# Performance work log

Measured on AMD Instinct MI355X. Metric: run time of the kernel, lower is better.

Reference implementation:

```python
import jax, jax.numpy as jnp
import numpy as np

N_NODES = 200000
N_EDGES = 400000
N_FEAT = 78
DIM = 128
N_LAYERS = 5
N_GRAPHS = 8192
BN_EPS = 1e-5


def setup_inputs() -> dict:
    key = jax.random.key(0)
    ks = jax.random.split(key, 20)
    s = 0.05
    inp = {
        "x": jax.random.normal(ks[0], (N_NODES, N_FEAT), dtype=jnp.float32),
        "edge_index": jax.random.randint(ks[1], (2, N_EDGES), 0, N_NODES, dtype=jnp.int64),
        "batch": jnp.sort(jax.random.randint(ks[2], (N_NODES,), 0, N_GRAPHS, dtype=jnp.int64)),
        "percent": 0,
        # ini_embed: Linear(F,D), ReLU, Linear(D,D)
        "ini_w1": jax.random.normal(ks[3], (N_FEAT, DIM), dtype=jnp.float32) * s,
        "ini_b1": jnp.zeros((DIM,), dtype=jnp.float32),
        "ini_w2": jax.random.normal(ks[4], (DIM, DIM), dtype=jnp.float32) * s,
        "ini_b2": jnp.zeros((DIM,), dtype=jnp.float32),
        # per-layer GIN MLPs (stacked over layers)
        "gin_w1": jax.random.normal(ks[5], (N_LAYERS, DIM, DIM), dtype=jnp.float32) * s,
        "gin_b1": jnp.zeros((N_LAYERS, DIM), dtype=jnp.float32),
        "gin_w2": jax.random.normal(ks[6], (N_LAYERS, DIM, DIM), dtype=jnp.float32) * s,
        "gin_b2": jnp.zeros((N_LAYERS, DIM), dtype=jnp.float32),
        # BatchNorm1d params per layer
        "bn_gamma": jnp.ones((N_LAYERS, DIM), dtype=jnp.float32),
        "bn_beta": jnp.zeros((N_LAYERS, DIM), dtype=jnp.float32),
        # layer_conv: Conv2d(L, 1, (1,1)) == weighted sum over layer axis + scalar bias
        "lc_w": jax.random.normal(ks[7], (N_LAYERS,), dtype=jnp.float32) * s,
        "lc_b": jnp.zeros((), dtype=jnp.float32),
    }
    return inp


def reference(x, edge_index, batch, percent, ini_w1, ini_b1, ini_w2, ini_b2,
              gin_w1, gin_b1, gin_w2, gin_b2, bn_gamma, bn_beta, lc_w, lc_b):
    # ini_embed
    h = jax.nn.relu(x @ ini_w1 + ini_b1) @ ini_w2 + ini_b2  # [N, D]
    src, dst = edge_index[0], edge_index[1]

    layer_outs = []
    for i in range(N_LAYERS):
        # GINConv (eps=0): mlp(x_i + sum_{j->i} x_j)
        agg = jax.ops.segment_sum(h[src], dst, num_segments=N_NODES)  # scatter-add
        z = agg + h
        z = jax.nn.relu(z @ gin_w1[i] + gin_b1[i]) @ gin_w2[i] + gin_b2[i]
        z = jax.nn.relu(z)
        # BatchNorm1d (training-mode batch stats over nodes)
        mean = jnp.mean(z, axis=0)
        var = jnp.var(z, axis=0)
        z = (z - mean) * jax.lax.rsqrt(var + BN_EPS) * bn_gamma[i] + bn_beta[i]
        layer_outs.append(z)
        h = z

    stacked = jnp.stack(layer_outs, axis=1)  # [N, L, D]
    # layer_conv: 1x1 Conv2d over the layer channel axis
    pos_global_node = jnp.einsum('nld,l->nd', stacked, lc_w) + lc_b  # [N, D]
    # global_add_pool
    pos_global_graph = jax.ops.segment_sum(pos_global_node, batch, num_segments=N_GRAPHS)
    return pos_global_graph
```

## Files before the change

### kernel.cpp

```cpp
#include <hip/hip_runtime.h>

#define NN 200000
#define NE 400000
#define NFEAT 78
#define DIM 128
#define NLAYERS 5
#define NGRAPHS 8192
#define BN_EPS_C 1e-5f
#define NSLOT 32

typedef __attribute__((ext_vector_type(8))) short short8;
typedef __attribute__((ext_vector_type(8))) unsigned short ushort8;
typedef __attribute__((ext_vector_type(4))) float f32x4;

__device__ inline float bf2f(unsigned short u) {
    union { unsigned int i; float f; } c; c.i = ((unsigned int)u) << 16; return c.f;
}
__device__ inline unsigned short f2bf(float f) {
    union { float f; unsigned int i; } c; c.f = f;
    unsigned int x = c.i;
    x += 0x7FFFu + ((x >> 16) & 1u);
    return (unsigned short)(x >> 16);
}

template<int RELU2, int STATS>
__global__ __launch_bounds__(256, 4) void gin_mlp_kernel(
    const unsigned short* __restrict__ A,
    const unsigned short* __restrict__ W1d, const unsigned short* __restrict__ W2d,
    const float* __restrict__ b1, const float* __restrict__ b2,
    unsigned short* __restrict__ Z, float* __restrict__ stats_base)
{
    __shared__ unsigned short C1[128 * 128];

    int t = threadIdx.x;
    int r0 = blockIdx.x * 128;
    int lane = t & 63;
    int wv = t >> 6;
    int l15 = lane & 15;
    int lg = lane >> 4;

    float b1v[8], b2v[8];
#pragma unroll
    for (int nt = 0; nt < 8; ++nt) { b1v[nt] = b1[nt * 16 + l15]; b2v[nt] = b2[nt * 16 + l15]; }

    int ra0 = r0 + wv * 32 + l15;       if (ra0 > NN - 1) ra0 = NN - 1;
    int ra1 = r0 + wv * 32 + 16 + l15;  if (ra1 > NN - 1) ra1 = NN - 1;
    const unsigned short* __restrict__ Arow0 = A + (size_t)ra0 * DIM;
    const unsigned short* __restrict__ Arow1 = A + (size_t)ra1 * DIM;

    f32x4 zero4 = {0.f, 0.f, 0.f, 0.f};
    f32x4 acc[2][8];
#pragma unroll
    for (int mt = 0; mt < 2; ++mt)
#pragma unroll
        for (int nt = 0; nt < 8; ++nt) acc[mt][nt] = zero4;

#pragma unroll
    for (int ks = 0; ks < 4; ++ks) {
        int kgp = ks * 4 + lg;
        short8 a0 = *(const short8*)(Arow0 + kgp * 8);
        short8 a1 = *(const short8*)(Arow1 + kgp * 8);
#pragma unroll
        for (int nt = 0; nt < 8; ++nt) {
            short8 b = *(const short8*)(W1d + (size_t)(kgp * 128 + nt * 16 + l15) * 8);
            acc[0][nt] = __builtin_amdgcn_mfma_f32_16x16x32_bf16(a0, b, acc[0][nt], 0, 0, 0);
            acc[1][nt] = __builtin_amdgcn_mfma_f32_16x16x32_bf16(a1, b, acc[1][nt], 0, 0, 0);
        }
    }

#pragma unroll
    for (int mt = 0; mt < 2; ++mt)
#pragma unroll
        for (int nt = 0; nt < 8; ++nt)
#pragma unroll
            for (int rg = 0; rg < 4; ++rg) {
                int rr = wv * 32 + mt * 16 + lg * 4 + rg;
                int c = nt * 16 + l15;
                float v = fmaxf(acc[mt][nt][rg] + b1v[nt], 0.f);
                unsigned byte = (unsigned)((rr * 128 + c) * 2) ^ (unsigned)((rr & 7) << 4);
                *(unsigned short*)((char*)C1 + byte) = f2bf(v);
            }

    f32x4 acc2[2][8];
#pragma unroll
    for (int mt = 0; mt < 2; ++mt)
#pragma unroll
        for (int nt = 0; nt < 8; ++nt) acc2[mt][nt] = zero4;

#pragma unroll
    for (int ks = 0; ks < 4; ++ks) {
        int kgp = ks * 4 + lg;
        int m0 = wv * 32 + l15, m1 = m0 + 16;
        unsigned ba0 = (unsigned)(m0 * 256 + kgp * 16) ^ (unsigned)((m0 & 7) << 4);
        unsigned ba1 = (unsigned)(m1 * 256 + kgp * 16) ^ (unsigned)((m1 & 7) << 4);
        short8 a0 = *(const short8*)((char*)C1 + ba0);
        short8 a1 = *(const short8*)((char*)C1 + ba1);
#pragma unroll
        for (int nt = 0; nt < 8; ++nt) {
            short8 b = *(const short8*)(W2d + (size_t)(kgp * 128 + nt * 16 + l15) * 8);
            acc2[0][nt] = __builtin_amdgcn_mfma_f32_16x16x32_bf16(a0, b, acc2[0][nt], 0, 0, 0);
            acc2[1][nt] = __builtin_amdgcn_mfma_f32_16x16x32_bf16(a1, b, acc2[1][nt], 0, 0, 0);
        }
    }

#pragma unroll
    for (int nt = 0; nt < 8; ++nt) {
        float sum8 = 0.f, sq8 = 0.f;
        int c = nt * 16 + l15;
#pragma unroll
        for (int mt = 0; mt < 2; ++mt)
#pragma unroll
            for (int rg = 0; rg < 4; ++rg) {
                int rr = wv * 32 + mt * 16 + lg * 4 + rg;
                int r = r0 + rr;
                if (r < NN) {
                    float v = acc2[mt][nt][rg] + b2v[nt];
                    if (RELU2) v = fmaxf(v, 0.f);
                    Z[(size_t)r * DIM + c] = f2bf(v);
                    if (STATS) { sum8 += v; sq8 += v * v; }
                }
            }
        if (STATS) {
            sum8 += __shfl_xor(sum8, 16); sum8 += __shfl_xor(sum8, 32);
            sq8  += __shfl_xor(sq8, 16);  sq8  += __shfl_xor(sq8, 32);
            if (lg == 0) {
                float* sb = stats_base + (size_t)(blockIdx.x & (NSLOT - 1)) * 256;
                atomicAdd(&sb[c], sum8);
                atomicAdd(&sb[128 + c], sq8);
            }
        }
    }
}

__global__ __launch_bounds__(256) void wconv_kernel(
    const float* __restrict__ ini_w1, const float* __restrict__ ini_w2,
    const float* __restrict__ gw1, const float* __restrict__ gw2,
    unsigned short* __restrict__ Wd)
{
    int id = blockIdx.x * 256 + threadIdx.x;
    int k = id >> 7, n = id & 127;
    int y = blockIdx.y;
    float v;
    if (y == 0)      v = (k < NFEAT) ? ini_w1[k * DIM + n] : 0.f;
    else if (y == 1) v = ini_w2[k * DIM + n];
    else if (y < 7)  v = gw1[(size_t)(y - 2) * DIM * DIM + k * DIM + n];
    else             v = gw2[(size_t)(y - 7) * DIM * DIM + k * DIM + n];
    int kg = k >> 3;
    Wd[(size_t)y * 16384 + (size_t)(kg * 128 + n) * 8 + (k & 7)] = f2bf(v);
}

__global__ __launch_bounds__(256) void xpad_kernel(
    const float* __restrict__ x, unsigned short* __restrict__ xp)
{
    int t = blockIdx.x * 256 + threadIdx.x;
    int n = t >> 4, j = t & 15;
    ushort8 o;
#pragma unroll
    for (int i = 0; i < 8; ++i) {
        int c = j * 8 + i;
        o[i] = (c < NFEAT) ? f2bf(x[(size_t)n * NFEAT + c]) : (unsigned short)0;
    }
    *(ushort8*)(xp + (size_t)n * DIM + j * 8) = o;
}

__global__ __launch_bounds__(256) void deg_kernel(const int* __restrict__ ei, int* __restrict__ deg)
{
    int e = blockIdx.x * 256 + threadIdx.x;
    if (e >= NE) return;
    atomicAdd(&deg[ei[NE + e]], 1);
}

__global__ __launch_bounds__(256) void scanA_kernel(
    const int* __restrict__ deg, int* __restrict__ cursor, int* __restrict__ partials)
{
    __shared__ int sh[256];
    int i = blockIdx.x * 256 + threadIdx.x;
    int v = (i < NN) ? deg[i] : 0;
    sh[threadIdx.x] = v;
    __syncthreads();
    for (int off = 1; off < 256; off <<= 1) {
        int t2 = (threadIdx.x >= off) ? sh[threadIdx.x - off] : 0;
        __syncthreads();
        sh[threadIdx.x] += t2;
        __syncthreads();
    }
    int incl = sh[threadIdx.x];
    if (i < NN) cursor[i] = incl - v;
    if (threadIdx.x == 255) partials[blockIdx.x] = incl;
}

__global__ __launch_bounds__(1024) void scanB_kernel(int* __restrict__ partials, int nb)
{
    __shared__ int sh[1024];
    int i = threadIdx.x;
    int v = (i < nb) ? partials[i] : 0;
    sh[i] = v;
    __syncthreads();
    for (int off = 1; off < 1024; off <<= 1) {
        int t2 = (i >= off) ? sh[i - off] : 0;
        __syncthreads();
        sh[i] += t2;
        __syncthreads();
    }
    if (i < nb) partials[i] = sh[i] - v;
}

__global__ __launch_bounds__(256) void scanC_kernel(
    int* __restrict__ cursor, const int* __restrict__ partials)
{
    int i = blockIdx.x * 256 + threadIdx.x;
    if (i < NN) cursor[i] += partials[blockIdx.x];
}

__global__ __launch_bounds__(256) void fill_kernel(
    const int* __restrict__ ei, int* __restrict__ cursor, int* __restrict__ csr_src)
{
    int e = blockIdx.x * 256 + threadIdx.x;
    if (e >= NE) return;
    int slot = atomicAdd(&cursor[ei[NE + e]], 1);
    csr_src[slot] = ei[e];
}

__global__ __launch_bounds__(256) void gptr_kernel(
    const int* __restrict__ batch, int* __restrict__ gptr)
{
    int n = blockIdx.x * 256 + threadIdx.x;
    if (n > NN) return;
    int b1 = (n < NN) ? batch[n] : NGRAPHS;
    int b0 = (n == 0) ? -1 : batch[n - 1];
    for (int g = b0 + 1; g <= b1; ++g) gptr[g] = n;
}

__global__ void ident_kernel(float* __restrict__ aff)
{
    int d = threadIdx.x;
    aff[d] = 1.f;
    aff[DIM + d] = 0.f;
}

__global__ __launch_bounds__(256) void gather_kernel(
    const unsigned short* __restrict__ z, const int* __restrict__ cursor,
    const int* __restrict__ csr_src, const float* __restrict__ aff,
    unsigned short* __restrict__ agg)
{
    int t = blockIdx.x * 256 + threadIdx.x;
    int n = t >> 4, j = t & 15;
    int end = cursor[n];
    int beg = (n == 0) ? 0 : cursor[n - 1];
    ushort8 sv = *(const ushort8*)(z + (size_t)n * DIM + j * 8);
    float a[8];
#pragma unroll
    for (int i = 0; i < 8; ++i) a[i] = bf2f(sv[i]);
    for (int e = beg; e < end; ++e) {
        int s = csr_src[e];
        ushort8 v = *(const ushort8*)(z + (size_t)s * DIM + j * 8);
#pragma unroll
        for (int i = 0; i < 8; ++i) a[i] += bf2f(v[i]);
    }
    float cnt = (float)(end - beg + 1);
    ushort8 o;
#pragma unroll
    for (int i = 0; i < 8; ++i) {
        float av = aff[j * 8 + i];
        float cv = aff[DIM + j * 8 + i];
        o[i] = f2bf(fmaf(av, a[i], cnt * cv));
    }
    *(ushort8*)(agg + (size_t)n * DIM + j * 8) = o;
}

__global__ __launch_bounds__(128) void pool_kernel(
    const unsigned short* __restrict__ z, const int* __restrict__ gptr,
    const float* __restrict__ aff, const float* __restrict__ lcw, int l,
    const float* __restrict__ lcb_p, int add_lcb, float* __restrict__ out)
{
    int g = blockIdx.x;
    int d = threadIdx.x;
    int p0 = gptr[g], p1 = gptr[g + 1];
    float S = 0.f;
    for (int n = p0; n < p1; ++n) S += bf2f(z[(size_t)n * DIM + d]);
    float w = lcw[l];
    float cnt = (float)(p1 - p0);
    float v = w * fmaf(aff[d], S, cnt * aff[DIM + d]);
    if (add_lcb) v = fmaf(cnt, *lcb_p, v);
    out[(size_t)g * DIM + d] += v;
}

__global__ void finalize_kernel(
    const float* __restrict__ slots, const float* __restrict__ gamma,
    const float* __restrict__ beta, float* __restrict__ aff)
{
    int d = threadIdx.x;
    float s = 0.f, sq = 0.f;
    for (int i = 0; i < NSLOT; ++i) {
        s  += slots[i * 256 + d];
        sq += slots[i * 256 + 128 + d];
    }
    float mean = s * (1.0f / NN);
    float var = sq * (1.0f / NN) - mean * mean;
    float a = gamma[d] * rsqrtf(var + BN_EPS_C);
    aff[d] = a;
    aff[DIM + d] = beta[d] - mean * a;
}

extern "C" void kernel_launch(void* const* d_in, const int* in_sizes, int n_in,
                              void* d_out, int out_size, void* d_ws, size_t ws_size,
                              hipStream_t stream)
{
    const float* x      = (const float*)d_in[0];
    const int*   ei     = (const int*)d_in[1];
    const int*   batch  = (const int*)d_in[2];
    const float* ini_w1 = (const float*)d_in[4];
    const float* ini_b1 = (const float*)d_in[5];
    const float* ini_w2 = (const float*)d_in[6];
    const float* ini_b2 = (const float*)d_in[7];
    const float* gw1    = (const float*)d_in[8];
    const float* gb1    = (const float*)d_in[9];
    const float* gw2    = (const float*)d_in[10];
    const float* gb2    = (const float*)d_in[11];
    const float* gamma  = (const float*)d_in[12];
    const float* beta   = (const float*)d_in[13];
    const float* lcw    = (const float*)d_in[14];
    const float* lcb    = (const float*)d_in[15];
    float* out = (float*)d_out;

    size_t NHs = (size_t)NN * DIM;
    unsigned short* bufA = (unsigned short*)d_ws;
    unsigned short* bufB = bufA + NHs;
    unsigned short* Wd   = bufB + NHs;
    float* stats  = (float*)(Wd + 12 * 16384);
    float* affine = stats + (size_t)NLAYERS * NSLOT * 256;
    int* deg      = (int*)(affine + (NLAYERS + 1) * 256);
    int* cursor   = deg + NN;
    int* csr_src  = cursor + NN;
    int* partials = csr_src + NE;
    int* gptr     = partials + 1024;
    size_t need = (size_t)((char*)(gptr + NGRAPHS + 1) - (char*)d_ws);

    hipMemsetAsync(out, 0, (size_t)NGRAPHS * DIM * sizeof(float), stream);
    if (ws_size < need) return;

    hipMemsetAsync(stats, 0, (size_t)NLAYERS * NSLOT * 256 * sizeof(float), stream);
    hipMemsetAsync(deg, 0, NN * sizeof(int), stream);

    int nb = (NN + 255) / 256;
    int eb = (NE + 255) / 256;

    deg_kernel<<<eb, 256, 0, stream>>>(ei, deg);
    scanA_kernel<<<nb, 256, 0, stream>>>(deg, cursor, partials);
    scanB_kernel<<<1, 1024, 0, stream>>>(partials, nb);
    scanC_kernel<<<nb, 256, 0, stream>>>(cursor, partials);
    fill_kernel<<<eb, 256, 0, stream>>>(ei, cursor, csr_src);
    gptr_kernel<<<(NN + 256) / 256 + 1, 256, 0, stream>>>(batch, gptr);
    ident_kernel<<<1, 128, 0, stream>>>(affine);

    xpad_kernel<<<NN * 16 / 256, 256, 0, stream>>>(x, bufB);
    wconv_kernel<<<dim3(64, 12), 256, 0, stream>>>(ini_w1, ini_w2, gw1, gw2, Wd);

    int gin_blocks = (NN + 127) / 128;

    gin_mlp_kernel<0, 0><<<gin_blocks, 256, 0, stream>>>(
        bufB, Wd, Wd + 16384, ini_b1, ini_b2, bufA, nullptr);

    unsigned short* prev = bufA;
    for (int l = 0; l < NLAYERS; ++l) {
        unsigned short* nxt = (prev == bufA) ? bufB : bufA;
        gather_kernel<<<NN * 16 / 256, 256, 0, stream>>>(
            prev, cursor, csr_src, affine + (size_t)l * 256, nxt);
        gin_mlp_kernel<1, 1><<<gin_blocks, 256, 0, stream>>>(
            nxt, Wd + (size_t)(2 + l) * 16384, Wd + (size_t)(7 + l) * 16384,
            gb1 + l * DIM, gb2 + l * DIM, nxt, stats + (size_t)l * NSLOT * 256);
        finalize_kernel<<<1, 128, 0, stream>>>(
            stats + (size_t)l * NSLOT * 256, gamma + l * DIM, beta + l * DIM,
            affine + (size_t)(l + 1) * 256);
        pool_kernel<<<NGRAPHS, 128, 0, stream>>>(
            nxt, gptr, affine + (size_t)(l + 1) * 256, lcw, l, lcb,
            (l == 0) ? 1 : 0, out);
        prev = nxt;
    }
}
```

Baseline: 754.5 us.

## Fuse neighbor gather into GIN MLP kernel with LDS-staged coalesced stores

The separate gather kernel is removed. Each MLP block now computes the neighbor aggregation and BN affine for its 128-row tile directly into shared memory and feeds it to the first MFMA GEMM. This avoids writing and re-reading the aggregated bf16 activations in global memory every layer. The output tile is also staged through the swizzled LDS buffer so the final stores are 16-byte coalesced. Each block processes two tiles, so fewer blocks run and the irregular gather latency is no longer overlapped by a separate, highly parallel kernel.

```diff
diff --git a/kernel.cpp b/kernel.cpp
--- a/kernel.cpp
+++ b/kernel.cpp
@@ -8,6 +8,7 @@
 #define NGRAPHS 8192
 #define BN_EPS_C 1e-5f
 #define NSLOT 32
+#define NTILES 1563
 
 typedef __attribute__((ext_vector_type(8))) short short8;
 typedef __attribute__((ext_vector_type(8))) unsigned short ushort8;
@@ -23,17 +24,18 @@
     return (unsigned short)(x >> 16);
 }
 
-template<int RELU2, int STATS>
-__global__ __launch_bounds__(256, 4) void gin_mlp_kernel(
+template<int GATHERM, int RELU2, int STATS>
+__global__ __launch_bounds__(256, 4) void gin_fused_kernel(
     const unsigned short* __restrict__ A,
+    const int* __restrict__ cursor, const int* __restrict__ csr_src,
+    const float* __restrict__ aff,
     const unsigned short* __restrict__ W1d, const unsigned short* __restrict__ W2d,
     const float* __restrict__ b1, const float* __restrict__ b2,
     unsigned short* __restrict__ Z, float* __restrict__ stats_base)
 {
-    __shared__ unsigned short C1[128 * 128];
+    __shared__ unsigned short S[128 * 128];
 
     int t = threadIdx.x;
-    int r0 = blockIdx.x * 128;
     int lane = t & 63;
     int wv = t >> 6;
     int l15 = lane & 15;
@@ -43,90 +45,156 @@
 #pragma unroll
     for (int nt = 0; nt < 8; ++nt) { b1v[nt] = b1[nt * 16 + l15]; b2v[nt] = b2[nt * 16 + l15]; }
 
-    int ra0 = r0 + wv * 32 + l15;       if (ra0 > NN - 1) ra0 = NN - 1;
-    int ra1 = r0 + wv * 32 + 16 + l15;  if (ra1 > NN - 1) ra1 = NN - 1;
-    const unsigned short* __restrict__ Arow0 = A + (size_t)ra0 * DIM;
-    const unsigned short* __restrict__ Arow1 = A + (size_t)ra1 * DIM;
-
-    f32x4 zero4 = {0.f, 0.f, 0.f, 0.f};
-    f32x4 acc[2][8];
-#pragma unroll
-    for (int mt = 0; mt < 2; ++mt)
-#pragma unroll
-        for (int nt = 0; nt < 8; ++nt) acc[mt][nt] = zero4;
-
-#pragma unroll
-    for (int ks = 0; ks < 4; ++ks) {
-        int kgp = ks * 4 + lg;
-        short8 a0 = *(const short8*)(Arow0 + kgp * 8);
-        short8 a1 = *(const short8*)(Arow1 + kgp * 8);
+    float av[8], cv[8];
+    if (GATHERM) {
+        int j = t & 15;
+#pragma unroll
+        for (int i = 0; i < 8; ++i) { av[i] = aff[j * 8 + i]; cv[i] = aff[DIM + j * 8 + i]; }
+    }
+
+    for (int tile = blockIdx.x * 2; tile < blockIdx.x * 2 + 2; ++tile) {
+        if (tile >= NTILES) break;
+        int r0 = tile * 128;
+
+        if (GATHERM) {
+            if (tile != blockIdx.x * 2) __syncthreads();
+            int j = t & 15;
+#pragma unroll
+            for (int it = 0; it < 8; ++it) {
+                int lr = it * 16 + (t >> 4);
+                int n = r0 + lr;
+                ushort8 o;
+                if (n < NN) {
+                    int end = cursor[n];
+                    int beg = (n == 0) ? 0 : cursor[n - 1];
+                    ushort8 sv = *(const ushort8*)(A + (size_t)n * DIM + j * 8);
+                    float acc[8];
+#pragma unroll
+                    for (int i = 0; i < 8; ++i) acc[i] = bf2f(sv[i]);
+                    for (int e = beg; e < end; ++e) {
+                        int s = csr_src[e];
+                        ushort8 v = *(const ushort8*)(A + (size_t)s * DIM + j * 8);
+#pragma unroll
+                        for (int i = 0; i < 8; ++i) acc[i] += bf2f(v[i]);
+                    }
+                    float cnt = (float)(end - beg + 1);
+#pragma unroll
+                    for (int i = 0; i < 8; ++i) o[i] = f2bf(fmaf(av[i], acc[i], cnt * cv[i]));
+                } else {
+#pragma unroll
+                    for (int i = 0; i < 8; ++i) o[i] = 0;
+                }
+                unsigned byte = (unsigned)(lr * 256 + j * 16) ^ (unsigned)((lr & 7) << 4);
+                *(ushort8*)((char*)S + byte) = o;
+            }
+            __syncthreads();
+        }
+
+        int ra0 = r0 + wv * 32 + l15;       if (ra0 > NN - 1) ra0 = NN - 1;
+        int ra1 = r0 + wv * 32 + 16 + l15;  if (ra1 > NN - 1) ra1 = NN - 1;
+        const unsigned short* Arow0 = A + (size_t)ra0 * DIM;
+        const unsigned short* Arow1 = A + (size_t)ra1 * DIM;
+
+        f32x4 zero4 = {0.f, 0.f, 0.f, 0.f};
+        f32x4 acc[2][8];
+#pragma unroll
+        for (int mt = 0; mt < 2; ++mt)
+#pragma unroll
+            for (int nt = 0; nt < 8; ++nt) acc[mt][nt] = zero4;
+
+#pragma unroll
+        for (int ks = 0; ks < 4; ++ks) {
+            int kgp = ks * 4 + lg;
+            short8 a0, a1;
+            if (GATHERM) {
+                int m0 = wv * 32 + l15, m1 = m0 + 16;
+                unsigned ba0 = (unsigned)(m0 * 256 + kgp * 16) ^ (unsigned)((m0 & 7) << 4);
+                unsigned ba1 = (unsigned)(m1 * 256 + kgp * 16) ^ (unsigned)((m1 & 7) << 4);
+                a0 = *(const short8*)((char*)S + ba0);
+                a1 = *(const short8*)((char*)S + ba1);
+            } else {
+                a0 = *(const short8*)(Arow0 + kgp * 8);
+                a1 = *(const short8*)(Arow1 + kgp * 8);
+            }
+#pragma unroll
+            for (int nt = 0; nt < 8; ++nt) {
+                short8 b = *(const short8*)(W1d + (size_t)(kgp * 128 + nt * 16 + l15) * 8);
+                acc[0][nt] = __builtin_amdgcn_mfma_f32_16x16x32_bf16(a0, b, acc[0][nt], 0, 0, 0);
+                acc[1][nt] = __builtin_amdgcn_mfma_f32_16x16x32_bf16(a1, b, acc[1][nt], 0, 0, 0);
+            }
+        }
+
+#pragma unroll
+        for (int mt = 0; mt < 2; ++mt)
+#pragma unroll
+            for (int nt = 0; nt < 8; ++nt)
+#pragma unroll
+                for (int rg = 0; rg < 4; ++rg) {
+                    int rr = wv * 32 + mt * 16 + lg * 4 + rg;
+                    int c = nt * 16 + l15;
+                    float v = fmaxf(acc[mt][nt][rg] + b1v[nt], 0.f);
+                    unsigned byte = (unsigned)(rr * 256 + c * 2) ^ (unsigned)((rr & 7) << 4);
+                    *(unsigned short*)((char*)S + byte) = f2bf(v);
+                }
+
+        f32x4 acc2[2][8];
+#pragma unroll
+        for (int mt = 0; mt < 2; ++mt)
+#pragma unroll
+            for (int nt = 0; nt < 8; ++nt) acc2[mt][nt] = zero4;
+
+#pragma unroll
+        for (int ks = 0; ks < 4; ++ks) {
+            int kgp = ks * 4 + lg;
+            int m0 = wv * 32 + l15, m1 = m0 + 16;
+            unsigned ba0 = (unsigned)(m0 * 256 + kgp * 16) ^ (unsigned)((m0 & 7) << 4);
+            unsigned ba1 = (unsigned)(m1 * 256 + kgp * 16) ^ (unsigned)((m1 & 7) << 4);
+            short8 a0 = *(const short8*)((char*)S + ba0);
+            short8 a1 = *(const short8*)((char*)S + ba1);
+#pragma unroll
+            for (int nt = 0; nt < 8; ++nt) {
+                short8 b = *(const short8*)(W2d + (size_t)(kgp * 128 + nt * 16 + l15) * 8);
+                acc2[0][nt] = __builtin_amdgcn_mfma_f32_16x16x32_bf16(a0, b, acc2[0][nt], 0, 0, 0);
+                acc2[1][nt] = __builtin_amdgcn_mfma_f32_16x16x32_bf16(a1, b, acc2[1][nt], 0, 0, 0);
+            }
+        }
+
 #pragma unroll
         for (int nt = 0; nt < 8; ++nt) {
-            short8 b = *(const short8*)(W1d + (size_t)(kgp * 128 + nt * 16 + l15) * 8);
-            acc[0][nt] = __builtin_amdgcn_mfma_f32_16x16x32_bf16(a0, b, acc[0][nt], 0, 0, 0);
-            acc[1][nt] = __builtin_amdgcn_mfma_f32_16x16x32_bf16(a1, b, acc[1][nt], 0, 0, 0);
-        }
-    }
-
-#pragma unroll
-    for (int mt = 0; mt < 2; ++mt)
-#pragma unroll
-        for (int nt = 0; nt < 8; ++nt)
-#pragma unroll
-            for (int rg = 0; rg < 4; ++rg) {
-                int rr = wv * 32 + mt * 16 + lg * 4 + rg;
-                int c = nt * 16 + l15;
-                float v = fmaxf(acc[mt][nt][rg] + b1v[nt], 0.f);
-                unsigned byte = (unsigned)((rr * 128 + c) * 2) ^ (unsigned)((rr & 7) << 4);
-                *(unsigned short*)((char*)C1 + byte) = f2bf(v);
-            }
-
-    f32x4 acc2[2][8];
-#pragma unroll
-    for (int mt = 0; mt < 2; ++mt)
-#pragma unroll
-        for (int nt = 0; nt < 8; ++nt) acc2[mt][nt] = zero4;
-
-#pragma unroll
-    for (int ks = 0; ks < 4; ++ks) {
-        int kgp = ks * 4 + lg;
-        int m0 = wv * 32 + l15, m1 = m0 + 16;
-        unsigned ba0 = (unsigned)(m0 * 256 + kgp * 16) ^ (unsigned)((m0 & 7) << 4);
-        unsigned ba1 = (unsigned)(m1 * 256 + kgp * 16) ^ (unsigned)((m1 & 7) << 4);
-        short8 a0 = *(const short8*)((char*)C1 + ba0);
-        short8 a1 = *(const short8*)((char*)C1 + ba1);
-#pragma unroll
-        for (int nt = 0; nt < 8; ++nt) {
-            short8 b = *(const short8*)(W2d + (size_t)(kgp * 128 + nt * 16 + l15) * 8);
-            acc2[0][nt] = __builtin_amdgcn_mfma_f32_16x16x32_bf16(a0, b, acc2[0][nt], 0, 0, 0);
-            acc2[1][nt] = __builtin_amdgcn_mfma_f32_16x16x32_bf16(a1, b, acc2[1][nt], 0, 0, 0);
-        }
-    }
-
-#pragma unroll
-    for (int nt = 0; nt < 8; ++nt) {
-        float sum8 = 0.f, sq8 = 0.f;
-        int c = nt * 16 + l15;
-#pragma unroll
-        for (int mt = 0; mt < 2; ++mt)
-#pragma unroll
-            for (int rg = 0; rg < 4; ++rg) {
-                int rr = wv * 32 + mt * 16 + lg * 4 + rg;
-                int r = r0 + rr;
-                if (r < NN) {
+            float sum8 = 0.f, sq8 = 0.f;
+            int c = nt * 16 + l15;
+#pragma unroll
+            for (int mt = 0; mt < 2; ++mt)
+#pragma unroll
+                for (int rg = 0; rg < 4; ++rg) {
+                    int rr = wv * 32 + mt * 16 + lg * 4 + rg;
                     float v = acc2[mt][nt][rg] + b2v[nt];
                     if (RELU2) v = fmaxf(v, 0.f);
-                    Z[(size_t)r * DIM + c] = f2bf(v);
-                    if (STATS) { sum8 += v; sq8 += v * v; }
+                    unsigned byte = (unsigned)(rr * 256 + c * 2) ^ (unsigned)((rr & 7) << 4);
+                    *(unsigned short*)((char*)S + byte) = f2bf(v);
+                    if (STATS && (r0 + rr < NN)) { sum8 += v; sq8 += v * v; }
                 }
-            }
-        if (STATS) {
-            sum8 += __shfl_xor(sum8, 16); sum8 += __shfl_xor(sum8, 32);
-            sq8  += __shfl_xor(sq8, 16);  sq8  += __shfl_xor(sq8, 32);
-            if (lg == 0) {
-                float* sb = stats_base + (size_t)(blockIdx.x & (NSLOT - 1)) * 256;
-                atomicAdd(&sb[c], sum8);
-                atomicAdd(&sb[128 + c], sq8);
+            if (STATS) {
+                sum8 += __shfl_xor(sum8, 16); sum8 += __shfl_xor(sum8, 32);
+                sq8  += __shfl_xor(sq8, 16);  sq8  += __shfl_xor(sq8, 32);
+                if (lg == 0) {
+                    float* sb = stats_base + (size_t)(tile & (NSLOT - 1)) * 256;
+                    atomicAdd(&sb[c], sum8);
+                    atomicAdd(&sb[128 + c], sq8);
+                }
+            }
+        }
+
+#pragma unroll
+        for (int st = 0; st < 8; ++st) {
+            int idx = st * 64 + lane;
+            int lr2 = wv * 32 + (idx >> 4);
+            int j2 = idx & 15;
+            int r = r0 + lr2;
+            if (r < NN) {
+                unsigned byte = (unsigned)(lr2 * 256 + j2 * 16) ^ (unsigned)((lr2 & 7) << 4);
+                ushort8 v = *(const ushort8*)((char*)S + byte);
+                *(ushort8*)(Z + (size_t)r * DIM + j2 * 8) = v;
             }
         }
     }
@@ -236,36 +304,6 @@
     int d = threadIdx.x;
     aff[d] = 1.f;
     aff[DIM + d] = 0.f;
-}
-
-__global__ __launch_bounds__(256) void gather_kernel(
-    const unsigned short* __restrict__ z, const int* __restrict__ cursor,
-    const int* __restrict__ csr_src, const float* __restrict__ aff,
-    unsigned short* __restrict__ agg)
-{
-    int t = blockIdx.x * 256 + threadIdx.x;
-    int n = t >> 4, j = t & 15;
-    int end = cursor[n];
-    int beg = (n == 0) ? 0 : cursor[n - 1];
-    ushort8 sv = *(const ushort8*)(z + (size_t)n * DIM + j * 8);
-    float a[8];
-#pragma unroll
-    for (int i = 0; i < 8; ++i) a[i] = bf2f(sv[i]);
-    for (int e = beg; e < end; ++e) {
-        int s = csr_src[e];
-        ushort8 v = *(const ushort8*)(z + (size_t)s * DIM + j * 8);
-#pragma unroll
-        for (int i = 0; i < 8; ++i) a[i] += bf2f(v[i]);
-    }
-    float cnt = (float)(end - beg + 1);
-    ushort8 o;
-#pragma unroll
-    for (int i = 0; i < 8; ++i) {
-        float av = aff[j * 8 + i];
-        float cv = aff[DIM + j * 8 + i];
-        o[i] = f2bf(fmaf(av, a[i], cnt * cv));
-    }
-    *(ushort8*)(agg + (size_t)n * DIM + j * 8) = o;
 }
 
 __global__ __launch_bounds__(128) void pool_kernel(
@@ -356,18 +394,17 @@
     xpad_kernel<<<NN * 16 / 256, 256, 0, stream>>>(x, bufB);
     wconv_kernel<<<dim3(64, 12), 256, 0, stream>>>(ini_w1, ini_w2, gw1, gw2, Wd);
 
-    int gin_blocks = (NN + 127) / 128;
-
-    gin_mlp_kernel<0, 0><<<gin_blocks, 256, 0, stream>>>(
-        bufB, Wd, Wd + 16384, ini_b1, ini_b2, bufA, nullptr);
+    int fused_blocks = (NTILES + 1) / 2;
+
+    gin_fused_kernel<0, 0, 0><<<fused_blocks, 256, 0, stream>>>(
+        bufB, nullptr, nullptr, nullptr, Wd, Wd + 16384, ini_b1, ini_b2, bufA, nullptr);
 
     unsigned short* prev = bufA;
     for (int l = 0; l < NLAYERS; ++l) {
         unsigned short* nxt = (prev == bufA) ? bufB : bufA;
-        gather_kernel<<<NN * 16 / 256, 256, 0, stream>>>(
-            prev, cursor, csr_src, affine + (size_t)l * 256, nxt);
-        gin_mlp_kernel<1, 1><<<gin_blocks, 256, 0, stream>>>(
-            nxt, Wd + (size_t)(2 + l) * 16384, Wd + (size_t)(7 + l) * 16384,
+        gin_fused_kernel<1, 1, 1><<<fused_blocks, 256, 0, stream>>>(
+            prev, cursor, csr_src, affine + (size_t)l * 256,
+            Wd + (size_t)(2 + l) * 16384, Wd + (size_t)(7 + l) * 16384,
             gb1 + l * DIM, gb2 + l * DIM, nxt, stats + (size_t)l * NSLOT * 256);
         finalize_kernel<<<1, 128, 0, stream>>>(
             stats + (size_t)l * NSLOT * 256, gamma + l * DIM, beta + l * DIM,
```

After: 2.555 ms. 3.39x slower.

## Restructure GIN MLP kernel to single-wave blocks with LDS-staged vector stores

Applied to the files above, without the earlier changes.

Each fused two-layer MLP block now holds one 64-thread wave that handles 32 rows as two sequential 16-row tiles, instead of four waves over 128 rows. The shared intermediate buffer shrinks from 32KB to 4KB, and accumulator register pressure is halved, which should allow more resident blocks per CU. Output is staged through swizzled LDS and written with 16-byte vector stores rather than scattered 2-byte stores. The trade-offs are more blocks to schedule, more atomics for BN statistics, and no bounds guard on rows, which relies on NN being a multiple of 32.

```diff
diff --git a/kernel.cpp b/kernel.cpp
--- a/kernel.cpp
+++ b/kernel.cpp
@@ -24,110 +24,103 @@
 }
 
 template<int RELU2, int STATS>
-__global__ __launch_bounds__(256, 4) void gin_mlp_kernel(
+__global__ __launch_bounds__(64, 6) void gin_mlp_kernel(
     const unsigned short* __restrict__ A,
     const unsigned short* __restrict__ W1d, const unsigned short* __restrict__ W2d,
     const float* __restrict__ b1, const float* __restrict__ b2,
     unsigned short* __restrict__ Z, float* __restrict__ stats_base)
 {
-    __shared__ unsigned short C1[128 * 128];
-
-    int t = threadIdx.x;
-    int r0 = blockIdx.x * 128;
-    int lane = t & 63;
-    int wv = t >> 6;
+    __shared__ unsigned short S[16 * 128];
+
+    int lane = threadIdx.x;
     int l15 = lane & 15;
     int lg = lane >> 4;
+    int r0 = blockIdx.x * 32;
 
     float b1v[8], b2v[8];
 #pragma unroll
     for (int nt = 0; nt < 8; ++nt) { b1v[nt] = b1[nt * 16 + l15]; b2v[nt] = b2[nt * 16 + l15]; }
 
-    int ra0 = r0 + wv * 32 + l15;       if (ra0 > NN - 1) ra0 = NN - 1;
-    int ra1 = r0 + wv * 32 + 16 + l15;  if (ra1 > NN - 1) ra1 = NN - 1;
-    const unsigned short* __restrict__ Arow0 = A + (size_t)ra0 * DIM;
-    const unsigned short* __restrict__ Arow1 = A + (size_t)ra1 * DIM;
-
     f32x4 zero4 = {0.f, 0.f, 0.f, 0.f};
-    f32x4 acc[2][8];
-#pragma unroll
-    for (int mt = 0; mt < 2; ++mt)
-#pragma unroll
-        for (int nt = 0; nt < 8; ++nt) acc[mt][nt] = zero4;
-
-#pragma unroll
-    for (int ks = 0; ks < 4; ++ks) {
-        int kgp = ks * 4 + lg;
-        short8 a0 = *(const short8*)(Arow0 + kgp * 8);
-        short8 a1 = *(const short8*)(Arow1 + kgp * 8);
+
+#pragma unroll
+    for (int mt = 0; mt < 2; ++mt) {
+        const unsigned short* __restrict__ Arow = A + (size_t)(r0 + mt * 16 + l15) * DIM;
+
+        f32x4 acc[8];
+#pragma unroll
+        for (int nt = 0; nt < 8; ++nt) acc[nt] = zero4;
+
+#pragma unroll
+        for (int ks = 0; ks < 4; ++ks) {
+            int kgp = ks * 4 + lg;
+            short8 a = *(const short8*)(Arow + kgp * 8);
+#pragma unroll
+            for (int nt = 0; nt < 8; ++nt) {
+                short8 b = *(const short8*)(W1d + (size_t)(kgp * 128 + nt * 16 + l15) * 8);
+                acc[nt] = __builtin_amdgcn_mfma_f32_16x16x32_bf16(a, b, acc[nt], 0, 0, 0);
+            }
+        }
+
+#pragma unroll
+        for (int nt = 0; nt < 8; ++nt)
+#pragma unroll
+            for (int rg = 0; rg < 4; ++rg) {
+                int lr = lg * 4 + rg;
+                int c = nt * 16 + l15;
+                float v = fmaxf(acc[nt][rg] + b1v[nt], 0.f);
+                unsigned byte = (unsigned)(lr * 256 + c * 2) ^ (unsigned)((lr & 7) << 4);
+                *(unsigned short*)((char*)S + byte) = f2bf(v);
+            }
+
+        f32x4 acc2[8];
+#pragma unroll
+        for (int nt = 0; nt < 8; ++nt) acc2[nt] = zero4;
+
+#pragma unroll
+        for (int ks = 0; ks < 4; ++ks) {
+            int kgp = ks * 4 + lg;
+            unsigned ba = (unsigned)(l15 * 256 + kgp * 16) ^ (unsigned)((l15 & 7) << 4);
+            short8 a = *(const short8*)((char*)S + ba);
+#pragma unroll
+            for (int nt = 0; nt < 8; ++nt) {
+                short8 b = *(const short8*)(W2d + (size_t)(kgp * 128 + nt * 16 + l15) * 8);
+                acc2[nt] = __builtin_amdgcn_mfma_f32_16x16x32_bf16(a, b, acc2[nt], 0, 0, 0);
+            }
+        }
+
 #pragma unroll
         for (int nt = 0; nt < 8; ++nt) {
-            short8 b = *(const short8*)(W1d + (size_t)(kgp * 128 + nt * 16 + l15) * 8);
-            acc[0][nt] = __builtin_amdgcn_mfma_f32_16x16x32_bf16(a0, b, acc[0][nt], 0, 0, 0);
-            acc[1][nt] = __builtin_amdgcn_mfma_f32_16x16x32_bf16(a1, b, acc[1][nt], 0, 0, 0);
+            float sum8 = 0.f, sq8 = 0.f;
+            int c = nt * 16 + l15;
+#pragma unroll
+            for (int rg = 0; rg < 4; ++rg) {
+                int lr = lg * 4 + rg;
+                float v = acc2[nt][rg] + b2v[nt];
+                if (RELU2) v = fmaxf(v, 0.f);
+                unsigned byte = (unsigned)(lr * 256 + c * 2) ^ (unsigned)((lr & 7) << 4);
+                *(unsigned short*)((char*)S + byte) = f2bf(v);
+                if (STATS) { sum8 += v; sq8 += v * v; }
+            }
+            if (STATS) {
+                sum8 += __shfl_xor(sum8, 16); sum8 += __shfl_xor(sum8, 32);
+                sq8  += __shfl_xor(sq8, 16);  sq8  += __shfl_xor(sq8, 32);
+                if (lg == 0) {
+                    float* sb = stats_base + (size_t)(blockIdx.x & (NSLOT - 1)) * 256;
+                    atomicAdd(&sb[c], sum8);
+                    atomicAdd(&sb[128 + c], sq8);
+                }
+            }
         }
-    }
-
-#pragma unroll
-    for (int mt = 0; mt < 2; ++mt)
-#pragma unroll
-        for (int nt = 0; nt < 8; ++nt)
-#pragma unroll
-            for (int rg = 0; rg < 4; ++rg) {
-                int rr = wv * 32 + mt * 16 + lg * 4 + rg;
-                int c = nt * 16 + l15;
-                float v = fmaxf(acc[mt][nt][rg] + b1v[nt], 0.f);
-                unsigned byte = (unsigned)((rr * 128 + c) * 2) ^ (unsigned)((rr & 7) << 4);
-                *(unsigned short*)((char*)C1 + byte) = f2bf(v);
-            }
-
-    f32x4 acc2[2][8];
-#pragma unroll
-    for (int mt = 0; mt < 2; ++mt)
-#pragma unroll
-        for (int nt = 0; nt < 8; ++nt) acc2[mt][nt] = zero4;
-
-#pragma unroll
-    for (int ks = 0; ks < 4; ++ks) {
-        int kgp = ks * 4 + lg;
-        int m0 = wv * 32 + l15, m1 = m0 + 16;
-        unsigned ba0 = (unsigned)(m0 * 256 + kgp * 16) ^ (unsigned)((m0 & 7) << 4);
-        unsigned ba1 = (unsigned)(m1 * 256 + kgp * 16) ^ (unsigned)((m1 & 7) << 4);
-        short8 a0 = *(const short8*)((char*)C1 + ba0);
-        short8 a1 = *(const short8*)((char*)C1 + ba1);
-#pragma unroll
-        for (int nt = 0; nt < 8; ++nt) {
-            short8 b = *(const short8*)(W2d + (size_t)(kgp * 128 + nt * 16 + l15) * 8);
-            acc2[0][nt] = __builtin_amdgcn_mfma_f32_16x16x32_bf16(a0, b, acc2[0][nt], 0, 0, 0);
-            acc2[1][nt] = __builtin_amdgcn_mfma_f32_16x16x32_bf16(a1, b, acc2[1][nt], 0, 0, 0);
-        }
-    }
-
-#pragma unroll
-    for (int nt = 0; nt < 8; ++nt) {
-        float sum8 = 0.f, sq8 = 0.f;
-        int c = nt * 16 + l15;
-#pragma unroll
-        for (int mt = 0; mt < 2; ++mt)
-#pragma unroll
-            for (int rg = 0; rg < 4; ++rg) {
-                int rr = wv * 32 + mt * 16 + lg * 4 + rg;
-                int r = r0 + rr;
-                if (r < NN) {
-                    float v = acc2[mt][nt][rg] + b2v[nt];
-                    if (RELU2) v = fmaxf(v, 0.f);
-                    Z[(size_t)r * DIM + c] = f2bf(v);
-                    if (STATS) { sum8 += v; sq8 += v * v; }
-                }
-            }
-        if (STATS) {
-            sum8 += __shfl_xor(sum8, 16); sum8 += __shfl_xor(sum8, 32);
-            sq8  += __shfl_xor(sq8, 16);  sq8  += __shfl_xor(sq8, 32);
-            if (lg == 0) {
-                float* sb = stats_base + (size_t)(blockIdx.x & (NSLOT - 1)) * 256;
-                atomicAdd(&sb[c], sum8);
-                atomicAdd(&sb[128 + c], sq8);
-            }
+
+#pragma unroll
+        for (int st = 0; st < 4; ++st) {
+            int idx = st * 64 + lane;
+            int lr = idx >> 4;
+            int j = idx & 15;
+            unsigned byte = (unsigned)(lr * 256 + j * 16) ^ (unsigned)((lr & 7) << 4);
+            ushort8 v = *(const ushort8*)((char*)S + byte);
+            *(ushort8*)(Z + (size_t)(r0 + mt * 16 + lr) * DIM + j * 8) = v;
         }
     }
 }
@@ -356,9 +349,9 @@
     xpad_kernel<<<NN * 16 / 256, 256, 0, stream>>>(x, bufB);
     wconv_kernel<<<dim3(64, 12), 256, 0, stream>>>(ini_w1, ini_w2, gw1, gw2, Wd);
 
-    int gin_blocks = (NN + 127) / 128;
-
-    gin_mlp_kernel<0, 0><<<gin_blocks, 256, 0, stream>>>(
+    int gin_blocks = NN / 32;
+
+    gin_mlp_kernel<0, 0><<<gin_blocks, 64, 0, stream>>>(
         bufB, Wd, Wd + 16384, ini_b1, ini_b2, bufA, nullptr);
 
     unsigned short* prev = bufA;
@@ -366,7 +359,7 @@
         unsigned short* nxt = (prev == bufA) ? bufB : bufA;
         gather_kernel<<<NN * 16 / 256, 256, 0, stream>>>(
             prev, cursor, csr_src, affine + (size_t)l * 256, nxt);
-        gin_mlp_kernel<1, 1><<<gin_blocks, 256, 0, stream>>>(
+        gin_mlp_kernel<1, 1><<<gin_blocks, 64, 0, stream>>>(
             nxt, Wd + (size_t)(2 + l) * 16384, Wd + (size_t)(7 + l) * 16384,
             gb1 + l * DIM, gb2 + l * DIM, nxt, stats + (size_t)l * NSLOT * 256);
         finalize_kernel<<<1, 128, 0, stream>>>(
```

Result: slower. 1.066 ms (+41.3%).
